# Optimization experiments

Hardware: AMD Instinct MI355X
Metric: run time of the kernel (lower is better)

Reference implementation:

```python
import jax, jax.numpy as jnp
import numpy as np

N_HEAD = 12


def setup_inputs() -> dict:
    key = jax.random.key(0)
    k1, k2, k3 = jax.random.split(key, 3)
    B, T, C = 1, 4096, 768
    x = jax.random.normal(k1, (B, T, C), dtype=jnp.float32)
    w_attn = jax.random.normal(k2, (C, 3 * C), dtype=jnp.float32) * (1.0 / np.sqrt(C))
    w_proj = jax.random.normal(k3, (C, C), dtype=jnp.float32) * (1.0 / np.sqrt(C))
    return {"x": x, "w_attn": w_attn, "w_proj": w_proj}


def reference(x, w_attn, w_proj):
    B, T, C = x.shape
    hd = C // N_HEAD
    qkv = x @ w_attn  # [B, T, 3C]
    q, k, v = jnp.split(qkv, 3, axis=-1)
    # [B, H, T, hd]
    q = q.reshape(B, T, N_HEAD, hd).transpose(0, 2, 1, 3)
    k = k.reshape(B, T, N_HEAD, hd).transpose(0, 2, 1, 3)
    v = v.reshape(B, T, N_HEAD, hd).transpose(0, 2, 1, 3)
    scale = 1.0 / np.sqrt(hd).astype(np.float32)
    att = jnp.einsum('bhtd,bhsd->bhts', q, k) * scale  # materialized TxT scores
    causal = jnp.tril(jnp.ones((T, T), dtype=bool))
    att = jnp.where(causal[None, None], att, -jnp.inf)
    att = jax.nn.softmax(att, axis=-1)
    y = jnp.einsum('bhts,bhsd->bhtd', att, v)  # [B, H, T, hd]
    y = y.transpose(0, 2, 1, 3).reshape(B, T, C)
    return y @ w_proj
```

## Files before the change

kernel.cpp:

```cpp
#include <hip/hip_runtime.h>


typedef short bf16x8 __attribute__((ext_vector_type(8)));
typedef float f32x4 __attribute__((ext_vector_type(4)));

#define T_SEQ 4096
#define C_DIM 768
#define NH 12
#define HD 64

__device__ __forceinline__ unsigned short f2bf(float f) {
  union { float f; unsigned u; } v; v.f = f;
  unsigned r = v.u + 0x7FFFu + ((v.u >> 16) & 1u);
  return (unsigned short)(r >> 16);
}
__device__ __forceinline__ float bf2f(unsigned short u) {
  union { unsigned u; float f; } v; v.u = ((unsigned)u) << 16;
  return v.f;
}
__device__ __forceinline__ unsigned cvtpk(float a, float b) {
  unsigned r;
  asm("v_cvt_pk_bf16_f32 %0, %1, %2" : "=v"(r) : "v"(a), "v"(b));
  return r;
}

#define GLD16(g, l) __builtin_amdgcn_global_load_lds( \
    (const __attribute__((address_space(1))) void*)(g), \
    (__attribute__((address_space(3))) void*)(l), 16, 0, 0)

__global__ void conv_bf16(const float* __restrict__ in, unsigned short* __restrict__ out, int n) {
  int i = (blockIdx.x * blockDim.x + threadIdx.x) * 4;
  if (i + 3 < n) {
    float4 v = *reinterpret_cast<const float4*>(in + i);
    ushort4 o;
    o.x = f2bf(v.x); o.y = f2bf(v.y); o.z = f2bf(v.z); o.w = f2bf(v.w);
    *reinterpret_cast<ushort4*>(out + i) = o;
  }
}

__global__ void transpose_bf16(const float* __restrict__ in, unsigned short* __restrict__ out,
                               int R, int Cc) {
  __shared__ float tile[32][33];
  int bx = blockIdx.x * 32;
  int by = blockIdx.y * 32;
  int tx = threadIdx.x & 31, ty = threadIdx.x >> 5;
#pragma unroll
  for (int i = 0; i < 32; i += 8)
    tile[ty + i][tx] = in[(size_t)(by + ty + i) * Cc + bx + tx];
  __syncthreads();
#pragma unroll
  for (int i = 0; i < 32; i += 8)
    out[(size_t)(bx + ty + i) * R + by + tx] = f2bf(tile[tx][ty + i]);
}

template <int MODE>
__global__ __launch_bounds__(256, 2)
void gemm_bt(const unsigned short* __restrict__ A,
             const unsigned short* __restrict__ Bt,
             void* __restrict__ out0,
             unsigned short* __restrict__ Kout,
             unsigned short* __restrict__ Vt,
             int M, int N, int K) {
  __shared__ __align__(16) unsigned short As[128 * 64];
  __shared__ __align__(16) unsigned short Bs[128 * 64];
  const int bm = blockIdx.x, bn = blockIdx.y;
  const int tid = threadIdx.x;
  const int wid = tid >> 6, lane = tid & 63;
  const int wr = wid >> 1, wc = wid & 1;
  const int lr = lane & 15;
  const int lk8 = (lane >> 4) * 8;

  f32x4 acc[4][4] = {};

  const int nk = K / 64;
  for (int kt = 0; kt < nk; ++kt) {
    __syncthreads();
    {
      const unsigned short* gA = A + (size_t)(bm * 128) * K + kt * 64;
      const unsigned short* gB = Bt + (size_t)(bn * 128) * K + kt * 64;
      int rsub = lane >> 3, csub = (lane & 7) * 8;
#pragma unroll
      for (int c = 0; c < 4; ++c) {
        int seg = wid * 4 + c;
        int row = seg * 8 + rsub;
        GLD16(gA + (size_t)row * K + csub, (char*)As + seg * 1024);
      }
#pragma unroll
      for (int c = 0; c < 4; ++c) {
        int seg = wid * 4 + c;
        int row = seg * 8 + rsub;
        GLD16(gB + (size_t)row * K + csub, (char*)Bs + seg * 1024);
      }
    }
    __syncthreads();
#pragma unroll
    for (int kk = 0; kk < 2; ++kk) {
      bf16x8 a[4], b[4];
      int lk = kk * 32 + lk8;
#pragma unroll
      for (int m = 0; m < 4; ++m)
        a[m] = *reinterpret_cast<const bf16x8*>(&As[(wr * 64 + m * 16 + lr) * 64 + lk]);
#pragma unroll
      for (int n = 0; n < 4; ++n)
        b[n] = *reinterpret_cast<const bf16x8*>(&Bs[(wc * 64 + n * 16 + lr) * 64 + lk]);
#pragma unroll
      for (int m = 0; m < 4; ++m)
#pragma unroll
        for (int n = 0; n < 4; ++n)
          acc[m][n] = __builtin_amdgcn_mfma_f32_16x16x32_bf16(a[m], b[n], acc[m][n], 0, 0, 0);
    }
  }

  const int row0 = bm * 128 + wr * 64;
  const int col0 = bn * 128 + wc * 64;
#pragma unroll
  for (int m = 0; m < 4; ++m)
#pragma unroll
    for (int n = 0; n < 4; ++n)
#pragma unroll
      for (int j = 0; j < 4; ++j) {
        int r = row0 + m * 16 + (lane >> 4) * 4 + j;
        int c = col0 + n * 16 + (lane & 15);
        float v = acc[m][n][j];
        if (MODE == 0) {
          if (c < 768)
            ((unsigned short*)out0)[(size_t)r * 768 + c] = f2bf(v * 0.125f);
          else if (c < 1536)
            Kout[(size_t)r * 768 + (c - 768)] = f2bf(v);
          else
            Vt[(size_t)(c - 1536) * M + r] = f2bf(v);
        } else {
          ((float*)out0)[(size_t)r * N + c] = v;
        }
      }
}

__device__ __forceinline__ void stage_kv(const unsigned short* __restrict__ Kb,
                                         const unsigned short* __restrict__ Vt,
                                         unsigned short* Kbuf, unsigned short* Vbuf,
                                         int h, int st, int wid, int lane) {
  const int cg = lane & 7, rsub = (lane >> 3) & 7;
  const unsigned short* gK = Kb + (size_t)(st * 64) * C_DIM + h * 64;
  const unsigned short* gV = Vt + (size_t)(h * 64) * T_SEQ + st * 64;
#pragma unroll
  for (int c = 0; c < 2; ++c) {
    int seg = wid * 2 + c;
    int row = seg * 8 + rsub;
    GLD16(gK + (size_t)row * C_DIM + (cg ^ rsub) * 8, (char*)Kbuf + seg * 1024);
    GLD16(gV + (size_t)row * T_SEQ + (cg ^ rsub) * 8, (char*)Vbuf + seg * 1024);
  }
}

__device__ __forceinline__ int part_off(int qb) {
  return (qb < 16) ? (qb - 8) * 2 : (qb < 24) ? 16 + (qb - 16) * 3 : 40 + (qb - 24) * 4;
}
__device__ __forceinline__ unsigned short* part_ptr(char* pA, char* pB, int set) {
  return (set < 768) ? (unsigned short*)(pA + (size_t)set * 16384)
                     : (unsigned short*)(pB + (size_t)(set - 768) * 16384);
}

__global__ __launch_bounds__(256, 3)
void attn_fwd(const unsigned short* __restrict__ Qb,
              const unsigned short* __restrict__ Kb,
              const unsigned short* __restrict__ Vt,
              unsigned short* __restrict__ Y,
              char* __restrict__ partA, char* __restrict__ partB,
              float* __restrict__ ml) {
  __shared__ __align__(16) unsigned short Ks[2][64 * 64];
  __shared__ __align__(16) unsigned short Vs[2][64 * 64];
  __shared__ __align__(16) unsigned short Ps[4][32 * 64];

  const int h = blockIdx.y;
  int qb = 0, ck = 0;
  {
    int idx = blockIdx.x;
    for (int q = 31; q >= 0; --q) {
      int nc = q / 8 + 1;
      if (idx < nc) { qb = q; ck = idx; break; }
      idx -= nc;
    }
  }
  const int nch = qb / 8 + 1;
  const int q0 = qb * 128;
  const int nst_total = q0 / 64 + 2;
  const int st0 = ck * 16;
  const int st1 = (st0 + 16 < nst_total) ? st0 + 16 : nst_total;

  const int tid = threadIdx.x;
  const int wid = tid >> 6, lane = tid & 63;
  const int l15 = lane & 15, g = lane >> 4;
  const int sw = l15 & 7;
  const int qw = q0 + wid * 32;

  bf16x8 qf[2][2];
#pragma unroll
  for (int m = 0; m < 2; ++m)
#pragma unroll
    for (int kk = 0; kk < 2; ++kk)
      qf[m][kk] = *reinterpret_cast<const bf16x8*>(
          &Qb[(size_t)(qw + m * 16 + l15) * C_DIM + h * 64 + kk * 32 + g * 8]);

  f32x4 o[2][4] = {};
  float mrow[2] = {-1e30f, -1e30f};
  float lsum[2] = {0.f, 0.f};

  stage_kv(Kb, Vt, Ks[0], Vs[0], h, st0, wid, lane);
  int cur = 0;

  for (int st = st0; st < st1; ++st) {
    if (st + 1 < st1) {
      stage_kv(Kb, Vt, Ks[cur ^ 1], Vs[cur ^ 1], h, st + 1, wid, lane);
      asm volatile("s_waitcnt vmcnt(4)" ::: "memory");
    } else {
      asm volatile("s_waitcnt vmcnt(0)" ::: "memory");
    }
    __builtin_amdgcn_s_barrier();

    const bool active = (st * 64) <= (qw + 31);
    if (active) {
      const unsigned short* K_ = Ks[cur];
      const unsigned short* V_ = Vs[cur];

      f32x4 sT[2][4] = {};
      __builtin_amdgcn_s_setprio(1);
#pragma unroll
      for (int kk = 0; kk < 2; ++kk) {
        bf16x8 kf[4];
#pragma unroll
        for (int n = 0; n < 4; ++n)
          kf[n] = *reinterpret_cast<const bf16x8*>(
              &K_[(n * 16 + l15) * 64 + (((kk * 4 + g) ^ sw) * 8)]);
#pragma unroll
        for (int m = 0; m < 2; ++m)
#pragma unroll
          for (int n = 0; n < 4; ++n)
            sT[m][n] = __builtin_amdgcn_mfma_f32_16x16x32_bf16(kf[n], qf[m][kk], sT[m][n], 0, 0, 0);
      }
      __builtin_amdgcn_s_setprio(0);

      unsigned short* Pw = Ps[wid];
#pragma unroll
      for (int m = 0; m < 2; ++m) {
        float vmax = -1e30f;
        if (st * 64 + 63 <= qw + m * 16) {
#pragma unroll
          for (int n = 0; n < 4; ++n)
#pragma unroll
            for (int jj = 0; jj < 4; ++jj) vmax = fmaxf(vmax, sT[m][n][jj]);
        } else {
          const int bound = (qw + m * 16 + l15) - st * 64;
#pragma unroll
          for (int n = 0; n < 4; ++n)
#pragma unroll
            for (int jj = 0; jj < 4; ++jj) {
              int sl = n * 16 + g * 4 + jj;
              float v = sT[m][n][jj];
              v = (sl <= bound) ? v : -1e30f;
              sT[m][n][jj] = v;
              vmax = fmaxf(vmax, v);
            }
        }
        vmax = fmaxf(vmax, __shfl_xor(vmax, 16, 64));
        vmax = fmaxf(vmax, __shfl_xor(vmax, 32, 64));
        const bool defer = (__all(vmax <= mrow[m] + 8.0f) != 0);
        const float mnew = defer ? mrow[m] : fmaxf(mrow[m], vmax);
        float ps = 0.f;
#pragma unroll
        for (int n = 0; n < 4; ++n)
#pragma unroll
          for (int jj = 0; jj < 4; ++jj) {
            float p = __expf(sT[m][n][jj] - mnew);
            sT[m][n][jj] = p;
            ps += p;
          }
        ps += __shfl_xor(ps, 16, 64);
        ps += __shfl_xor(ps, 32, 64);
        if (defer) {
          lsum[m] += ps;
        } else {
          float alpha = __expf(mrow[m] - mnew);
          lsum[m] = lsum[m] * alpha + ps;
          mrow[m] = mnew;
#pragma unroll
          for (int n2 = 0; n2 < 4; ++n2) o[m][n2] *= alpha;
        }
#pragma unroll
        for (int n = 0; n < 4; ++n) {
          uint2 pw;
          pw.x = cvtpk(sT[m][n][0], sT[m][n][1]);
          pw.y = cvtpk(sT[m][n][2], sT[m][n][3]);
          *reinterpret_cast<uint2*>(
              &Pw[(m * 16 + l15) * 64 + (((n * 2 + (g >> 1)) ^ sw) * 8) + (g & 1) * 4]) = pw;
        }
      }
      asm volatile("s_waitcnt lgkmcnt(0)" ::: "memory");

      __builtin_amdgcn_s_setprio(1);
#pragma unroll
      for (int ks = 0; ks < 2; ++ks) {
        bf16x8 vf[4], pf[2];
#pragma unroll
        for (int n2 = 0; n2 < 4; ++n2)
          vf[n2] = *reinterpret_cast<const bf16x8*>(
              &V_[(n2 * 16 + l15) * 64 + (((ks * 4 + g) ^ sw) * 8)]);
#pragma unroll
        for (int m = 0; m < 2; ++m)
          pf[m] = *reinterpret_cast<const bf16x8*>(
              &Pw[(m * 16 + l15) * 64 + (((ks * 4 + g) ^ sw) * 8)]);
#pragma unroll
        for (int m = 0; m < 2; ++m)
#pragma unroll
          for (int n2 = 0; n2 < 4; ++n2)
            o[m][n2] = __builtin_amdgcn_mfma_f32_16x16x32_bf16(vf[n2], pf[m], o[m][n2], 0, 0, 0);
      }
      __builtin_amdgcn_s_setprio(0);
    }
    asm volatile("" ::: "memory");
    __builtin_amdgcn_s_barrier();
    cur ^= 1;
  }

  if (nch == 1) {
#pragma unroll
    for (int m = 0; m < 2; ++m) {
      float inv = 1.0f / lsum[m];
      int qg = qw + m * 16 + l15;
#pragma unroll
      for (int n2 = 0; n2 < 4; ++n2) {
        uint2 yk;
        yk.x = cvtpk(o[m][n2][0] * inv, o[m][n2][1] * inv);
        yk.y = cvtpk(o[m][n2][2] * inv, o[m][n2][3] * inv);
        *reinterpret_cast<uint2*>(&Y[(size_t)qg * C_DIM + h * 64 + n2 * 16 + g * 4]) = yk;
      }
    }
  } else {
    const int set = h * 72 + part_off(qb) + ck;
    unsigned short* po = part_ptr(partA, partB, set);
#pragma unroll
    for (int m = 0; m < 2; ++m) {
      int qL = wid * 32 + m * 16 + l15;
#pragma unroll
      for (int n2 = 0; n2 < 4; ++n2) {
        uint2 pk;
        pk.x = cvtpk(o[m][n2][0], o[m][n2][1]);
        pk.y = cvtpk(o[m][n2][2], o[m][n2][3]);
        *reinterpret_cast<uint2*>(&po[qL * 64 + n2 * 16 + g * 4]) = pk;
      }
      if (g == 0) {
        ml[(size_t)set * 256 + qL * 2] = mrow[m];
        ml[(size_t)set * 256 + qL * 2 + 1] = lsum[m];
      }
    }
  }
}

__global__ __launch_bounds__(256)
void attn_combine(char* __restrict__ partA, char* __restrict__ partB,
                  const float* __restrict__ ml, unsigned short* __restrict__ Y) {
  const int qb = 8 + blockIdx.x;
  const int h = blockIdx.y;
  const int nch = qb / 8 + 1;
  const int set0 = h * 72 + part_off(qb);
  const int t = threadIdx.x;
  const int r = t >> 1, dh = (t & 1) * 32;

  float mi[4], li[4];
  float M = -1e30f;
  for (int i = 0; i < nch; ++i) {
    mi[i] = ml[(size_t)(set0 + i) * 256 + r * 2];
    li[i] = ml[(size_t)(set0 + i) * 256 + r * 2 + 1];
    M = fmaxf(M, mi[i]);
  }
  float L = 0.f;
  float O[32];
#pragma unroll
  for (int d = 0; d < 32; ++d) O[d] = 0.f;
  for (int i = 0; i < nch; ++i) {
    float w = __expf(mi[i] - M);
    L += li[i] * w;
    const unsigned short* po = part_ptr(partA, partB, set0 + i) + r * 64 + dh;
#pragma unroll
    for (int d4 = 0; d4 < 32; d4 += 4) {
      ushort4 v = *reinterpret_cast<const ushort4*>(po + d4);
      O[d4 + 0] += bf2f(v.x) * w;
      O[d4 + 1] += bf2f(v.y) * w;
      O[d4 + 2] += bf2f(v.z) * w;
      O[d4 + 3] += bf2f(v.w) * w;
    }
  }
  float inv = 1.0f / L;
  unsigned short* yp = Y + (size_t)(qb * 128 + r) * C_DIM + h * 64 + dh;
#pragma unroll
  for (int d4 = 0; d4 < 32; d4 += 4) {
    uint2 yk;
    yk.x = cvtpk(O[d4 + 0] * inv, O[d4 + 1] * inv);
    yk.y = cvtpk(O[d4 + 2] * inv, O[d4 + 3] * inv);
    *reinterpret_cast<uint2*>(yp + d4) = yk;
  }
}

extern "C" void kernel_launch(void* const* d_in, const int* in_sizes, int n_in,
                              void* d_out, int out_size, void* d_ws, size_t ws_size,
                              hipStream_t stream) {
  const float* x = (const float*)d_in[0];
  const float* w_attn = (const float*)d_in[1];
  const float* w_proj = (const float*)d_in[2];
  float* out = (float*)d_out;

  char* ws = (char*)d_ws;
  unsigned short* Xb   = (unsigned short*)(ws + 0);
  unsigned short* WaT  = (unsigned short*)(ws + 6291456);
  unsigned short* WpT  = (unsigned short*)(ws + 9830400);
  unsigned short* Qb   = (unsigned short*)(ws + 11010048);
  unsigned short* Kb   = (unsigned short*)(ws + 17301504);
  unsigned short* Vt   = (unsigned short*)(ws + 23592960);
  unsigned short* Yb   = (unsigned short*)(ws + 29884416);

  char* partA = (char*)d_out;
  char* partB = (char*)ws;
  float* mlp  = (float*)(ws + 6291456);

  conv_bf16<<<(T_SEQ * C_DIM / 4 + 255) / 256, 256, 0, stream>>>(x, Xb, T_SEQ * C_DIM);
  transpose_bf16<<<dim3(2304 / 32, 768 / 32), 256, 0, stream>>>(w_attn, WaT, 768, 2304);
  transpose_bf16<<<dim3(768 / 32, 768 / 32), 256, 0, stream>>>(w_proj, WpT, 768, 768);

  gemm_bt<0><<<dim3(T_SEQ / 128, 2304 / 128), 256, 0, stream>>>(
      Xb, WaT, (void*)Qb, Kb, Vt, T_SEQ, 2304, C_DIM);

  attn_fwd<<<dim3(80, NH), 256, 0, stream>>>(Qb, Kb, Vt, Yb, partA, partB, mlp);
  attn_combine<<<dim3(24, NH), 256, 0, stream>>>(partA, partB, mlp, Yb);

  gemm_bt<1><<<dim3(T_SEQ / 128, C_DIM / 128), 256, 0, stream>>>(
      Yb, WpT, (void*)out, nullptr, nullptr, T_SEQ, C_DIM, C_DIM);
}
```

Measured before the change: 145.9 us.

## Double-buffer GEMM LDS tiles and swizzle workgroups across XCDs

Gives the bf16 GEMM two LDS buffers so the next k-tile's global-to-LDS loads are issued before computing on the current tile, with vmcnt waits and raw barriers replacing the sync-load-sync pattern. Launches a 1D grid and remaps block indices so consecutive tiles land on the same XCD (assuming 8 XCDs), aiming for better L2 reuse. This doubles LDS per block (64KB), which may reduce occupancy below the launch-bounds target of 2 blocks/CU. The swizzle assumes the tile count is divisible by 8.

```diff
diff --git a/kernel.cpp b/kernel.cpp
--- a/kernel.cpp
+++ b/kernel.cpp
@@ -61,54 +61,65 @@
              unsigned short* __restrict__ Kout,
              unsigned short* __restrict__ Vt,
              int M, int N, int K) {
-  __shared__ __align__(16) unsigned short As[128 * 64];
-  __shared__ __align__(16) unsigned short Bs[128 * 64];
-  const int bm = blockIdx.x, bn = blockIdx.y;
+  __shared__ __align__(16) unsigned short As[2][128 * 64];
+  __shared__ __align__(16) unsigned short Bs[2][128 * 64];
+  const int nbn = N / 128;
+  const int nwg = (M / 128) * nbn;
+  const int cpx = nwg >> 3;
+  const int swz = ((int)blockIdx.x & 7) * cpx + ((int)blockIdx.x >> 3);
+  const int bm = swz / nbn, bn = swz % nbn;
+
   const int tid = threadIdx.x;
   const int wid = tid >> 6, lane = tid & 63;
   const int wr = wid >> 1, wc = wid & 1;
   const int lr = lane & 15;
   const int lk8 = (lane >> 4) * 8;
+  const int rsub = lane >> 3, csub = (lane & 7) * 8;
 
   f32x4 acc[4][4] = {};
-
   const int nk = K / 64;
+
+  auto STAGE = [&](int kt, int buf) {
+    const unsigned short* gA = A + (size_t)(bm * 128) * K + kt * 64;
+    const unsigned short* gB = Bt + (size_t)(bn * 128) * K + kt * 64;
+#pragma unroll
+    for (int c = 0; c < 4; ++c) {
+      int seg = wid * 4 + c;
+      int row = seg * 8 + rsub;
+      GLD16(gA + (size_t)row * K + csub, (char*)As[buf] + seg * 1024);
+      GLD16(gB + (size_t)row * K + csub, (char*)Bs[buf] + seg * 1024);
+    }
+  };
+
+  STAGE(0, 0);
+  int cur = 0;
   for (int kt = 0; kt < nk; ++kt) {
-    __syncthreads();
-    {
-      const unsigned short* gA = A + (size_t)(bm * 128) * K + kt * 64;
-      const unsigned short* gB = Bt + (size_t)(bn * 128) * K + kt * 64;
-      int rsub = lane >> 3, csub = (lane & 7) * 8;
-#pragma unroll
-      for (int c = 0; c < 4; ++c) {
-        int seg = wid * 4 + c;
-        int row = seg * 8 + rsub;
-        GLD16(gA + (size_t)row * K + csub, (char*)As + seg * 1024);
-      }
-#pragma unroll
-      for (int c = 0; c < 4; ++c) {
-        int seg = wid * 4 + c;
-        int row = seg * 8 + rsub;
-        GLD16(gB + (size_t)row * K + csub, (char*)Bs + seg * 1024);
-      }
-    }
-    __syncthreads();
+    if (kt + 1 < nk) {
+      STAGE(kt + 1, cur ^ 1);
+      asm volatile("s_waitcnt vmcnt(8)" ::: "memory");
+    } else {
+      asm volatile("s_waitcnt vmcnt(0)" ::: "memory");
+    }
+    __builtin_amdgcn_s_barrier();
 #pragma unroll
     for (int kk = 0; kk < 2; ++kk) {
       bf16x8 a[4], b[4];
       int lk = kk * 32 + lk8;
 #pragma unroll
       for (int m = 0; m < 4; ++m)
-        a[m] = *reinterpret_cast<const bf16x8*>(&As[(wr * 64 + m * 16 + lr) * 64 + lk]);
+        a[m] = *reinterpret_cast<const bf16x8*>(&As[cur][(wr * 64 + m * 16 + lr) * 64 + lk]);
 #pragma unroll
       for (int n = 0; n < 4; ++n)
-        b[n] = *reinterpret_cast<const bf16x8*>(&Bs[(wc * 64 + n * 16 + lr) * 64 + lk]);
+        b[n] = *reinterpret_cast<const bf16x8*>(&Bs[cur][(wc * 64 + n * 16 + lr) * 64 + lk]);
 #pragma unroll
       for (int m = 0; m < 4; ++m)
 #pragma unroll
         for (int n = 0; n < 4; ++n)
           acc[m][n] = __builtin_amdgcn_mfma_f32_16x16x32_bf16(a[m], b[n], acc[m][n], 0, 0, 0);
     }
+    asm volatile("" ::: "memory");
+    __builtin_amdgcn_s_barrier();
+    cur ^= 1;
   }
 
   const int row0 = bm * 128 + wr * 64;
@@ -424,12 +435,12 @@
   transpose_bf16<<<dim3(2304 / 32, 768 / 32), 256, 0, stream>>>(w_attn, WaT, 768, 2304);
   transpose_bf16<<<dim3(768 / 32, 768 / 32), 256, 0, stream>>>(w_proj, WpT, 768, 768);
 
-  gemm_bt<0><<<dim3(T_SEQ / 128, 2304 / 128), 256, 0, stream>>>(
+  gemm_bt<0><<<(T_SEQ / 128) * (2304 / 128), 256, 0, stream>>>(
       Xb, WaT, (void*)Qb, Kb, Vt, T_SEQ, 2304, C_DIM);
 
   attn_fwd<<<dim3(80, NH), 256, 0, stream>>>(Qb, Kb, Vt, Yb, partA, partB, mlp);
   attn_combine<<<dim3(24, NH), 256, 0, stream>>>(partA, partB, mlp, Yb);
 
-  gemm_bt<1><<<dim3(T_SEQ / 128, C_DIM / 128), 256, 0, stream>>>(
+  gemm_bt<1><<<(T_SEQ / 128) * (C_DIM / 128), 256, 0, stream>>>(
       Yb, WpT, (void*)out, nullptr, nullptr, T_SEQ, C_DIM, C_DIM);
 }
```

After: 161.4 us. +10.6%, slower.
